# Optimization experiments

Measured on AMD Instinct MI355X. Metric: run time of the kernel, lower is better.

The kernel has to match this reference:

```python
import math
import jax, jax.numpy as jnp
import numpy as np

L = 6          # num_spherical
EDGE_DIM = 64
N_EDGES = 2_000_000


def setup_inputs() -> dict:
    key = jax.random.key(0)
    k1, k2, k3 = jax.random.split(key, 3)
    local_env = jax.random.normal(k1, (N_EDGES, 2, 3), dtype=jnp.float32)
    pair_indices = jax.random.randint(k2, (N_EDGES, 2), 0, 50000, dtype=jnp.int64)
    kernel = jax.random.normal(k3, (L * L, EDGE_DIM), dtype=jnp.float32) * (1.0 / math.sqrt(L * L))
    bias = jnp.zeros((EDGE_DIM,), dtype=jnp.float32)
    return {"local_env": local_env, "pair_indices": pair_indices, "kernel": kernel, "bias": bias}


def _dfact(n):
    # double factorial n!! for odd n (n >= -1)
    return float(math.prod(range(1, n + 1, 2)))


def real_sph_harm(theta, phi, l_max):
    """Real spherical harmonics Y_lm(theta, phi) for l in [0, l_max), m in [-l, l].
    Returns array of shape (E, l_max**2), ordered (l, m=-l..l)."""
    x = jnp.cos(theta)          # (E,)
    s = jnp.sin(theta)          # (E,)
    # associated Legendre P_l^m(x) via standard recurrences (Condon-Shortley phase)
    P = {(0, 0): jnp.ones_like(x)}
    for m in range(1, l_max):
        P[(m, m)] = ((-1.0) ** m) * _dfact(2 * m - 1) * s ** m
    for m in range(0, l_max - 1):
        P[(m + 1, m)] = (2.0 * m + 1.0) * x * P[(m, m)]
    for m in range(0, l_max):
        for l in range(m + 2, l_max):
            P[(l, m)] = ((2.0 * l - 1.0) * x * P[(l - 1, m)] - (l + m - 1.0) * P[(l - 2, m)]) / (l - m)
    cols = []
    for l in range(l_max):
        for m in range(-l, l + 1):
            am = abs(m)
            K = math.sqrt((2 * l + 1) / (4.0 * math.pi) * math.factorial(l - am) / math.factorial(l + am))
            if m == 0:
                cols.append(K * P[(l, 0)])
            elif m > 0:
                cols.append(math.sqrt(2.0) * K * jnp.cos(m * phi) * P[(l, m)])
            else:
                cols.append(math.sqrt(2.0) * K * jnp.sin(am * phi) * P[(l, am)])
    return jnp.stack(cols, axis=-1)  # (E, l_max^2)


def reference(local_env, pair_indices, kernel, bias):
    env = local_env.reshape(-1, 2, 3)
    polar = env[:, 0]   # (E, 3) local polar axis
    edges = env[:, 1]   # (E, 3) edge vector
    # polar angle theta = atan2(|polar x edge|, polar . edge)
    dot_t = jnp.sum(polar * edges, axis=-1)
    cross_t = jnp.linalg.norm(jnp.cross(polar, edges), axis=-1)
    theta = jnp.arctan2(cross_t, dot_t)
    # azimuthal angle phi w.r.t. a fixed vertical reference direction
    # (source code's undefined `vetical`; fixed global z-axis used here)
    edges_proj = edges * jnp.cos(theta)[:, None]
    vertical = jnp.array([0.0, 0.0, 1.0], dtype=local_env.dtype)
    dot_p = jnp.sum(vertical * edges_proj, axis=-1)
    cross_p = jnp.linalg.norm(jnp.cross(polar, edges_proj), axis=-1)
    phi = jnp.arctan2(cross_p, dot_p)
    sph = real_sph_harm(theta, phi, L)          # (E, L^2)
    out = sph @ kernel + bias                   # (E, edge_dim)
    return out, pair_indices
```

## Files before the change

kernel.cpp:

```cpp
#include <hip/hip_runtime.h>
#include <math.h>

#define FOURPI 12.566370614359172

typedef _Float16 f16x8 __attribute__((ext_vector_type(8)));
typedef float    f32x4 __attribute__((ext_vector_type(4)));

__global__ __launch_bounds__(256) void sph_edge_kernel(
    const float* __restrict__ env,
    const float* __restrict__ Kmat,
    const float* __restrict__ bias,
    float* __restrict__ out,
    int N)
{
    __shared__ __align__(16) _Float16 Ylds[256 * 64];
    __shared__ __align__(16) float    Cbuf[4][16 * 68];

    const int tid  = threadIdx.x;
    const int lane = tid & 63;
    const int w    = tid >> 6;
    const int g    = lane >> 4;
    const int c    = lane & 15;
    const int base = blockIdx.x * 256;
    const int valid = (N - base < 256) ? (N - base) : 256;

    f16x8 Bf[4][2];
    #pragma unroll
    for (int nt = 0; nt < 4; ++nt) {
        #pragma unroll
        for (int kt = 0; kt < 2; ++kt) {
            #pragma unroll
            for (int j = 0; j < 8; ++j) {
                int k = kt * 32 + g * 8 + j;
                float v = (k < 36) ? Kmat[k * 64 + nt * 16 + c] : 0.f;
                Bf[nt][kt][j] = (_Float16)v;
            }
        }
    }
    float biasv[4];
    #pragma unroll
    for (int nt = 0; nt < 4; ++nt) biasv[nt] = bias[nt * 16 + c];

    float Y[36];
    if (tid < valid) {
        const float* p6 = env + (size_t)(base + tid) * 6;
        float2 v0 = *reinterpret_cast<const float2*>(p6);
        float2 v1 = *reinterpret_cast<const float2*>(p6 + 2);
        float2 v2 = *reinterpret_cast<const float2*>(p6 + 4);
        float px = v0.x, py = v0.y, pz = v1.x;
        float ex = v1.y, ey = v2.x, ez = v2.y;

        float dot_t = px*ex + py*ey + pz*ez;
        float cxv = py*ez - pz*ey;
        float cyv = pz*ex - px*ez;
        float czv = px*ey - py*ex;
        float cr2 = cxv*cxv + cyv*cyv + czv*czv;
        float cross_t = sqrtf(cr2);
        float r = sqrtf(dot_t*dot_t + cr2);
        float x = 1.f, s = 0.f;
        if (r > 0.f) { x = dot_t / r; s = cross_t / r; }

        float dp = ez * x;
        float cp = fabsf(x) * cross_t;
        float rp = sqrtf(dp*dp + cp*cp);
        float c1 = 1.f, s1 = 0.f;
        if (rp > 0.f) { c1 = dp / rp; s1 = cp / rp; }

        float tc = 2.f * c1;
        float cm1 = c1,            sm1 = s1;
        float cm2 = tc*cm1 - 1.f,  sm2 = tc*sm1;
        float cm3 = tc*cm2 - cm1,  sm3 = tc*sm2 - sm1;
        float cm4 = tc*cm3 - cm2,  sm4 = tc*sm3 - sm2;
        float cm5 = tc*cm4 - cm3,  sm5 = tc*sm4 - sm3;

        float s2 = s*s, s3 = s2*s, s4 = s2*s2, s5 = s4*s;
        float P10 = x;
        float P11 = -s;
        float P20 = 1.5f*x*x - 0.5f;
        float P21 = -3.f*x*s;
        float P22 = 3.f*s2;
        float P30 = (5.f*x*P20 - 2.f*P10) * (1.f/3.f);
        float P31 = (5.f*x*P21 - 3.f*P11) * 0.5f;
        float P32 = 5.f*x*P22;
        float P33 = -15.f*s3;
        float P40 = (7.f*x*P30 - 3.f*P20) * 0.25f;
        float P41 = (7.f*x*P31 - 4.f*P21) * (1.f/3.f);
        float P42 = (7.f*x*P32 - 5.f*P22) * 0.5f;
        float P43 = 7.f*x*P33;
        float P44 = 105.f*s4;
        float P50 = (9.f*x*P40 - 4.f*P30) * 0.2f;
        float P51 = (9.f*x*P41 - 5.f*P31) * 0.25f;
        float P52 = (9.f*x*P42 - 6.f*P32) * (1.f/3.f);
        float P53 = (9.f*x*P43 - 7.f*P33) * 0.5f;
        float P54 = 9.f*x*P44;
        float P55 = -945.f*s5;

        const float SQ2 = 1.4142135623730951f;
        const float K00 = (float)sqrt(1.0/FOURPI);
        const float K10 = (float)sqrt(3.0/FOURPI);
        const float K11 = (float)sqrt(3.0/FOURPI/2.0);
        const float K20 = (float)sqrt(5.0/FOURPI);
        const float K21 = (float)sqrt(5.0/FOURPI/6.0);
        const float K22 = (float)sqrt(5.0/FOURPI/24.0);
        const float K30 = (float)sqrt(7.0/FOURPI);
        const float K31 = (float)sqrt(7.0/FOURPI/12.0);
        const float K32 = (float)sqrt(7.0/FOURPI/120.0);
        const float K33 = (float)sqrt(7.0/FOURPI/720.0);
        const float K40 = (float)sqrt(9.0/FOURPI);
        const float K41 = (float)sqrt(9.0/FOURPI/20.0);
        const float K42 = (float)sqrt(9.0/FOURPI/360.0);
        const float K43 = (float)sqrt(9.0/FOURPI/5040.0);
        const float K44 = (float)sqrt(9.0/FOURPI/40320.0);
        const float K50 = (float)sqrt(11.0/FOURPI);
        const float K51 = (float)sqrt(11.0/FOURPI/30.0);
        const float K52 = (float)sqrt(11.0/FOURPI/840.0);
        const float K53 = (float)sqrt(11.0/FOURPI/20160.0);
        const float K54 = (float)sqrt(11.0/FOURPI/362880.0);
        const float K55 = (float)sqrt(11.0/FOURPI/3628800.0);

        Y[0]  = K00;
        Y[1]  = SQ2*K11*sm1*P11;
        Y[2]  = K10*P10;
        Y[3]  = SQ2*K11*cm1*P11;
        Y[4]  = SQ2*K22*sm2*P22;
        Y[5]  = SQ2*K21*sm1*P21;
        Y[6]  = K20*P20;
        Y[7]  = SQ2*K21*cm1*P21;
        Y[8]  = SQ2*K22*cm2*P22;
        Y[9]  = SQ2*K33*sm3*P33;
        Y[10] = SQ2*K32*sm2*P32;
        Y[11] = SQ2*K31*sm1*P31;
        Y[12] = K30*P30;
        Y[13] = SQ2*K31*cm1*P31;
        Y[14] = SQ2*K32*cm2*P32;
        Y[15] = SQ2*K33*cm3*P33;
        Y[16] = SQ2*K44*sm4*P44;
        Y[17] = SQ2*K43*sm3*P43;
        Y[18] = SQ2*K42*sm2*P42;
        Y[19] = SQ2*K41*sm1*P41;
        Y[20] = K40*P40;
        Y[21] = SQ2*K41*cm1*P41;
        Y[22] = SQ2*K42*cm2*P42;
        Y[23] = SQ2*K43*cm3*P43;
        Y[24] = SQ2*K44*cm4*P44;
        Y[25] = SQ2*K55*sm5*P55;
        Y[26] = SQ2*K54*sm4*P54;
        Y[27] = SQ2*K53*sm3*P53;
        Y[28] = SQ2*K52*sm2*P52;
        Y[29] = SQ2*K51*sm1*P51;
        Y[30] = K50*P50;
        Y[31] = SQ2*K51*cm1*P51;
        Y[32] = SQ2*K52*cm2*P52;
        Y[33] = SQ2*K53*cm3*P53;
        Y[34] = SQ2*K54*cm4*P54;
        Y[35] = SQ2*K55*cm5*P55;
    } else {
        #pragma unroll
        for (int i = 0; i < 36; ++i) Y[i] = 0.f;
    }

    {
        _Float16 yh[64];
        #pragma unroll
        for (int i = 0; i < 36; ++i) yh[i] = (_Float16)Y[i];
        #pragma unroll
        for (int i = 36; i < 64; ++i) yh[i] = (_Float16)0.f;
        #pragma unroll
        for (int s = 0; s < 8; ++s) {
            int slot = s ^ (tid & 7);
            *reinterpret_cast<f16x8*>(&Ylds[tid * 64 + slot * 8]) =
                *reinterpret_cast<const f16x8*>(&yh[s * 8]);
        }
    }
    __syncthreads();

    #pragma unroll
    for (int mt = 0; mt < 4; ++mt) {
        const int row = w * 64 + mt * 16 + c;
        const int sw  = row & 7;
        f16x8 a0 = *reinterpret_cast<const f16x8*>(&Ylds[row * 64 + ((0 + g) ^ sw) * 8]);
        f16x8 a1 = *reinterpret_cast<const f16x8*>(&Ylds[row * 64 + ((4 + g) ^ sw) * 8]);

        f32x4 acc[4];
        #pragma unroll
        for (int nt = 0; nt < 4; ++nt) {
            f32x4 a = {biasv[nt], biasv[nt], biasv[nt], biasv[nt]};
            a = __builtin_amdgcn_mfma_f32_16x16x32_f16(a0, Bf[nt][0], a, 0, 0, 0);
            a = __builtin_amdgcn_mfma_f32_16x16x32_f16(a1, Bf[nt][1], a, 0, 0, 0);
            acc[nt] = a;
        }

        #pragma unroll
        for (int nt = 0; nt < 4; ++nt) {
            #pragma unroll
            for (int r = 0; r < 4; ++r)
                Cbuf[w][(g * 4 + r) * 68 + nt * 16 + c] = acc[nt][r];
        }
        __builtin_amdgcn_wave_barrier();

        const int e_chunk = base + w * 64 + mt * 16;
        float4* ob = reinterpret_cast<float4*>(out) + (size_t)e_chunk * 16;
        #pragma unroll
        for (int i = 0; i < 4; ++i) {
            int f4    = i * 64 + lane;
            int e_loc = f4 >> 4;
            int c4    = f4 & 15;
            if (e_chunk + e_loc < N) {
                float4 v = *reinterpret_cast<const float4*>(
                    &Cbuf[w][e_loc * 68 + c4 * 4]);
                ob[f4] = v;
            }
        }
        __builtin_amdgcn_wave_barrier();
    }
}

__global__ __launch_bounds__(256) void idx_copy_kernel(
    const int4* __restrict__ idx, float* __restrict__ outp, int n4)
{
    int i = blockIdx.x * 256 + threadIdx.x;
    if (i < n4) {
        int4 v = idx[i];
        float4 f = make_float4((float)v.x, (float)v.y, (float)v.z, (float)v.w);
        reinterpret_cast<float4*>(outp)[i] = f;
    }
}

extern "C" void kernel_launch(void* const* d_in, const int* in_sizes, int n_in,
                              void* d_out, int out_size, void* d_ws, size_t ws_size,
                              hipStream_t stream) {
    const float* env  = (const float*)d_in[0];
    const int*   idx  = (const int*)d_in[1];
    const float* Kmat = (const float*)d_in[2];
    const float* bias = (const float*)d_in[3];
    float* out = (float*)d_out;

    int N = in_sizes[0] / 6;
    int nidx = in_sizes[1];

    int blocks = (N + 255) / 256;
    sph_edge_kernel<<<blocks, 256, 0, stream>>>(env, Kmat, bias, out, N);

    int n4 = nidx / 4;
    int iblocks = (n4 + 255) / 256;
    idx_copy_kernel<<<iblocks, 256, 0, stream>>>(
        (const int4*)idx, out + (size_t)N * 64, n4);
}
```

Baseline: 125.6 us.

## Fuse index copy into main kernel and alias output staging onto Y LDS

Drops the separate index-copy kernel. Each block of the spherical-harmonics kernel now converts its share of pair indices (128 int4 per block, matching 2 indices per edge) to float. The per-wave output staging buffer now reuses the Y shared-memory region after all A fragments are loaded into registers and a block barrier, shrinking LDS per block to allow more resident blocks. This removes one kernel launch and its tail, and may raise occupancy, at the cost of an extra __syncthreads and more live registers for the preloaded fragments.

```diff
diff --git a/kernel.cpp b/kernel.cpp
--- a/kernel.cpp
+++ b/kernel.cpp
@@ -8,13 +8,14 @@
 
 __global__ __launch_bounds__(256) void sph_edge_kernel(
     const float* __restrict__ env,
+    const int4*  __restrict__ idx4,
     const float* __restrict__ Kmat,
     const float* __restrict__ bias,
     float* __restrict__ out,
-    int N)
+    int N, int n4)
 {
-    __shared__ __align__(16) _Float16 Ylds[256 * 64];
-    __shared__ __align__(16) float    Cbuf[4][16 * 68];
+    __shared__ __align__(16) char U[32768];
+    _Float16* Ylds = reinterpret_cast<_Float16*>(U);
 
     const int tid  = threadIdx.x;
     const int lane = tid & 63;
@@ -23,6 +24,18 @@
     const int c    = lane & 15;
     const int base = blockIdx.x * 256;
     const int valid = (N - base < 256) ? (N - base) : 256;
+
+    float* Cbuf = reinterpret_cast<float*>(U) + w * 1088;
+
+    {
+        int i4 = blockIdx.x * 128 + tid;
+        if (tid < 128 && i4 < n4) {
+            int4 v = idx4[i4];
+            float4 f = make_float4((float)v.x, (float)v.y,
+                                   (float)v.z, (float)v.w);
+            reinterpret_cast<float4*>(out + (size_t)N * 64)[i4] = f;
+        }
+    }
 
     f16x8 Bf[4][2];
     #pragma unroll
@@ -174,19 +187,26 @@
     }
     __syncthreads();
 
+    f16x8 a0[4], a1[4];
     #pragma unroll
     for (int mt = 0; mt < 4; ++mt) {
         const int row = w * 64 + mt * 16 + c;
         const int sw  = row & 7;
-        f16x8 a0 = *reinterpret_cast<const f16x8*>(&Ylds[row * 64 + ((0 + g) ^ sw) * 8]);
-        f16x8 a1 = *reinterpret_cast<const f16x8*>(&Ylds[row * 64 + ((4 + g) ^ sw) * 8]);
-
+        a0[mt] = *reinterpret_cast<const f16x8*>(
+            &Ylds[row * 64 + ((0 + g) ^ sw) * 8]);
+        a1[mt] = *reinterpret_cast<const f16x8*>(
+            &Ylds[row * 64 + ((4 + g) ^ sw) * 8]);
+    }
+    __syncthreads();
+
+    #pragma unroll
+    for (int mt = 0; mt < 4; ++mt) {
         f32x4 acc[4];
         #pragma unroll
         for (int nt = 0; nt < 4; ++nt) {
             f32x4 a = {biasv[nt], biasv[nt], biasv[nt], biasv[nt]};
-            a = __builtin_amdgcn_mfma_f32_16x16x32_f16(a0, Bf[nt][0], a, 0, 0, 0);
-            a = __builtin_amdgcn_mfma_f32_16x16x32_f16(a1, Bf[nt][1], a, 0, 0, 0);
+            a = __builtin_amdgcn_mfma_f32_16x16x32_f16(a0[mt], Bf[nt][0], a, 0, 0, 0);
+            a = __builtin_amdgcn_mfma_f32_16x16x32_f16(a1[mt], Bf[nt][1], a, 0, 0, 0);
             acc[nt] = a;
         }
 
@@ -194,7 +214,7 @@
         for (int nt = 0; nt < 4; ++nt) {
             #pragma unroll
             for (int r = 0; r < 4; ++r)
-                Cbuf[w][(g * 4 + r) * 68 + nt * 16 + c] = acc[nt][r];
+                Cbuf[(g * 4 + r) * 68 + nt * 16 + c] = acc[nt][r];
         }
         __builtin_amdgcn_wave_barrier();
 
@@ -207,22 +227,11 @@
             int c4    = f4 & 15;
             if (e_chunk + e_loc < N) {
                 float4 v = *reinterpret_cast<const float4*>(
-                    &Cbuf[w][e_loc * 68 + c4 * 4]);
+                    &Cbuf[e_loc * 68 + c4 * 4]);
                 ob[f4] = v;
             }
         }
         __builtin_amdgcn_wave_barrier();
-    }
-}
-
-__global__ __launch_bounds__(256) void idx_copy_kernel(
-    const int4* __restrict__ idx, float* __restrict__ outp, int n4)
-{
-    int i = blockIdx.x * 256 + threadIdx.x;
-    if (i < n4) {
-        int4 v = idx[i];
-        float4 f = make_float4((float)v.x, (float)v.y, (float)v.z, (float)v.w);
-        reinterpret_cast<float4*>(outp)[i] = f;
     }
 }
 
@@ -236,13 +245,9 @@
     float* out = (float*)d_out;
 
     int N = in_sizes[0] / 6;
-    int nidx = in_sizes[1];
+    int n4 = in_sizes[1] / 4;
 
     int blocks = (N + 255) / 256;
-    sph_edge_kernel<<<blocks, 256, 0, stream>>>(env, Kmat, bias, out, N);
-
-    int n4 = nidx / 4;
-    int iblocks = (n4 + 255) / 256;
-    idx_copy_kernel<<<iblocks, 256, 0, stream>>>(
-        (const int4*)idx, out + (size_t)N * 64, n4);
+    sph_edge_kernel<<<blocks, 256, 0, stream>>>(
+        env, (const int4*)idx, Kmat, bias, out, N, n4);
 }
```

Measured after the change: 142.7 us. +13.6%, slower.
